# Kernel optimization log

Measured on AMD Instinct MI355X. Metric: run time of the kernel, lower is better.

The kernel has to match this reference:

```python
import jax, jax.numpy as jnp
import numpy as np

N_NODES = 50000
N_EDGES = 800000
DIM = 64
N_HEADS = 4


def setup_inputs() -> dict:
    key = jax.random.key(0)
    ks = jax.random.split(key, 7)
    x = jax.random.normal(ks[0], (N_NODES, DIM), dtype=jnp.float32)
    Wq = jax.random.normal(ks[1], (DIM, DIM), dtype=jnp.float32) / np.sqrt(DIM)
    Wk = jax.random.normal(ks[2], (DIM, DIM), dtype=jnp.float32) / np.sqrt(DIM)
    Wv = jax.random.normal(ks[3], (DIM, DIM), dtype=jnp.float32) / np.sqrt(DIM)
    Wo = jax.random.normal(ks[4], (DIM, DIM), dtype=jnp.float32) / np.sqrt(DIM)
    src = jax.random.randint(ks[5], (N_EDGES,), 0, N_NODES, dtype=jnp.int32)
    dst = jax.random.randint(ks[6], (N_EDGES,), 0, N_NODES, dtype=jnp.int32)
    return {"x": x, "Wq": Wq, "Wk": Wk, "Wv": Wv, "Wo": Wo, "src": src, "dst": dst}


def _scatter_softmax(scores, dst, n_nodes):
    # scores: [E, H]; per-destination-node softmax over incoming edges.
    m = jax.ops.segment_max(scores, dst, num_segments=n_nodes)  # [N, H]
    m = jnp.maximum(m, jnp.float32(-1e9))  # mirror the -1e9 init of the torch code
    ex = jnp.exp(scores - m[dst])  # [E, H]
    denom = jax.ops.segment_sum(ex, dst, num_segments=n_nodes)  # [N, H]
    return ex / (denom[dst] + 1e-9)


def reference(x, Wq, Wk, Wv, Wo, src, dst):
    N, D = x.shape
    H = N_HEADS
    Dh = D // H
    q = (x @ Wq).reshape(N, H, Dh)
    k = (x @ Wk).reshape(N, H, Dh)
    v = (x @ Wv).reshape(N, H, Dh)
    # per-edge attention logits: [E, H]
    scores = jnp.einsum("ehd,ehd->eh", q[dst], k[src]) / jnp.sqrt(jnp.float32(Dh))
    alpha = _scatter_softmax(scores, dst, N)  # [E, H]
    # weighted aggregation of source values onto destination nodes
    agg = jax.ops.segment_sum(alpha[:, :, None] * v[src], dst, num_segments=N)  # [N, H, Dh]
    return agg.reshape(N, D) @ Wo
```

## Files before the change

kernel.cpp:

```cpp
#include <hip/hip_runtime.h>
#include <math.h>

#define HEADS 4
#define DH 16
#define D 64
#define MAXDEG 64

typedef unsigned short ushort_t;
typedef unsigned int uint_t;

__device__ __forceinline__ float bf2f(ushort_t u) {
    return __uint_as_float(((uint_t)u) << 16);
}
__device__ __forceinline__ ushort_t f2bf(float f) {
    uint_t u = __float_as_uint(f);
    u = (u + 0x7FFFu + ((u >> 16) & 1u)) >> 16;
    return (ushort_t)u;
}
__device__ __forceinline__ float bflo(uint_t u) { return __uint_as_float(u << 16); }
__device__ __forceinline__ float bfhi(uint_t u) { return __uint_as_float(u & 0xFFFF0000u); }

__global__ __launch_bounds__(256) void qkv_scatter_kernel(
        const float* __restrict__ x,
        const float* __restrict__ Wq,
        const float* __restrict__ Wk,
        const float* __restrict__ Wv,
        ushort_t* __restrict__ qbf,
        ushort_t* __restrict__ kbf,
        ushort_t* __restrict__ vbf,
        const int* __restrict__ src,
        const int* __restrict__ dst,
        int* __restrict__ cursor,
        ushort_t* __restrict__ csr,
        int N, int E) {
    __shared__ ushort_t wq[D][D];
    __shared__ ushort_t wk[D][D];
    __shared__ ushort_t wv[D][D];
    __shared__ float xs[16][D];

    int tid = threadIdx.x;
    for (int i = tid; i < D * D; i += 256) {
        wq[i >> 6][i & 63] = f2bf(Wq[i]);
        wk[i >> 6][i & 63] = f2bf(Wk[i]);
        wv[i >> 6][i & 63] = f2bf(Wv[i]);
    }

    int c = tid & 63;
    int g = tid >> 6;
    int row = tid >> 4;
    int col4 = tid & 15;

    int ntiles = (N + 15) >> 4;
    for (int tile = blockIdx.x; tile < ntiles; tile += gridDim.x) {
        int n0t = tile * 16;
        __syncthreads();
        float4 xv = make_float4(0.f, 0.f, 0.f, 0.f);
        if (n0t + row < N) xv = *(const float4*)(x + (size_t)(n0t + row) * D + col4 * 4);
        *(float4*)&xs[row][col4 * 4] = xv;
        __syncthreads();

        float aq0=0,aq1=0,aq2=0,aq3=0, ak0=0,ak1=0,ak2=0,ak3=0, av0=0,av1=0,av2=0,av3=0;
#pragma unroll 8
        for (int d = 0; d < D; ++d) {
            float wqv = bf2f(wq[d][c]), wkv = bf2f(wk[d][c]), wvv = bf2f(wv[d][c]);
            float x0 = xs[g*4+0][d], x1 = xs[g*4+1][d], x2 = xs[g*4+2][d], x3 = xs[g*4+3][d];
            aq0 += x0*wqv; ak0 += x0*wkv; av0 += x0*wvv;
            aq1 += x1*wqv; ak1 += x1*wkv; av1 += x1*wvv;
            aq2 += x2*wqv; ak2 += x2*wkv; av2 += x2*wvv;
            aq3 += x3*wqv; ak3 += x3*wkv; av3 += x3*wvv;
        }
        int nb = n0t + g * 4;
        if (nb+0 < N) { qbf[(size_t)(nb+0)*D+c]=f2bf(aq0); kbf[(size_t)(nb+0)*D+c]=f2bf(ak0); vbf[(size_t)(nb+0)*D+c]=f2bf(av0); }
        if (nb+1 < N) { qbf[(size_t)(nb+1)*D+c]=f2bf(aq1); kbf[(size_t)(nb+1)*D+c]=f2bf(ak1); vbf[(size_t)(nb+1)*D+c]=f2bf(av1); }
        if (nb+2 < N) { qbf[(size_t)(nb+2)*D+c]=f2bf(aq2); kbf[(size_t)(nb+2)*D+c]=f2bf(ak2); vbf[(size_t)(nb+2)*D+c]=f2bf(av2); }
        if (nb+3 < N) { qbf[(size_t)(nb+3)*D+c]=f2bf(aq3); kbf[(size_t)(nb+3)*D+c]=f2bf(ak3); vbf[(size_t)(nb+3)*D+c]=f2bf(av3); }
    }

    {
        int e0 = (int)((long long)E * blockIdx.x / gridDim.x);
        int e1 = (int)((long long)E * (blockIdx.x + 1) / gridDim.x);
        for (int e = e0 + tid; e < e1; e += 256) {
            int d = dst[e];
            int s = src[e];
            int pos = atomicAdd(&cursor[d], 1);
            if (pos < MAXDEG) csr[(size_t)d * MAXDEG + pos] = (ushort_t)s;
        }
    }
}

__global__ __launch_bounds__(512) void attn_kernel(const ushort_t* __restrict__ qbf,
                                                   const ushort_t* __restrict__ kbf,
                                                   const ushort_t* __restrict__ vbf,
                                                   const ushort_t* __restrict__ csr,
                                                   const int* __restrict__ cursor,
                                                   const float* __restrict__ Wo,
                                                   float* __restrict__ out,
                                                   int N) {
    __shared__ float wo[D][D];
    __shared__ float aggsh[8][D];

    int tid = threadIdx.x;
    for (int i = tid; i < D * D; i += 512) wo[i >> 6][i & 63] = Wo[i];
    __syncthreads();

    int lane = tid & 63;
    int wave = tid >> 6;
    int node = blockIdx.x * 8 + wave;
    if (node >= N) return;

    int hp  = lane & 3;
    int el  = lane >> 2;
    int hd  = (lane & 31) >> 3;
    int par = lane >> 5;
    int dp2 = 2 * (lane & 31);

    int cnt = cursor[node]; if (cnt > MAXDEG) cnt = MAXDEG;
    const ushort_t* row = csr + (size_t)node * MAXDEG;

    float qr[16];
    {
        const uint4* qp = (const uint4*)(qbf + (size_t)node * D + hp * DH);
        uint4 qa = qp[0], qb = qp[1];
        qr[0]=bflo(qa.x);  qr[1]=bfhi(qa.x);  qr[2]=bflo(qa.y);  qr[3]=bfhi(qa.y);
        qr[4]=bflo(qa.z);  qr[5]=bfhi(qa.z);  qr[6]=bflo(qa.w);  qr[7]=bfhi(qa.w);
        qr[8]=bflo(qb.x);  qr[9]=bfhi(qb.x);  qr[10]=bflo(qb.y); qr[11]=bfhi(qb.y);
        qr[12]=bflo(qb.z); qr[13]=bfhi(qb.z); qr[14]=bflo(qb.w); qr[15]=bfhi(qb.w);
    }

    int s0=0, s1=0, s2=0, s3=0;
    float sc0=-1e30f, sc1=-1e30f, sc2=-1e30f, sc3=-1e30f;

#define PH1SB(sb, sv, scv)                                                      \
    if ((sb) * 16 < cnt) {                                                      \
        int eidx = (sb) * 16 + el;                                              \
        if (eidx < cnt) sv = row[eidx];                                         \
        const uint4* kp = (const uint4*)(kbf + (size_t)sv * D + hp * DH);       \
        uint4 ka = kp[0], kb = kp[1];                                           \
        float dot =                                                             \
          bflo(ka.x)*qr[0]  + bfhi(ka.x)*qr[1]                                  \
        + bflo(ka.y)*qr[2]  + bfhi(ka.y)*qr[3]                                  \
        + bflo(ka.z)*qr[4]  + bfhi(ka.z)*qr[5]                                  \
        + bflo(ka.w)*qr[6]  + bfhi(ka.w)*qr[7]                                  \
        + bflo(kb.x)*qr[8]  + bfhi(kb.x)*qr[9]                                  \
        + bflo(kb.y)*qr[10] + bfhi(kb.y)*qr[11]                                 \
        + bflo(kb.z)*qr[12] + bfhi(kb.z)*qr[13]                                 \
        + bflo(kb.w)*qr[14] + bfhi(kb.w)*qr[15];                                \
        scv = (eidx < cnt) ? dot * 0.25f : -1e30f;                              \
    }
    PH1SB(0, s0, sc0)
    PH1SB(1, s1, sc1)
    PH1SB(2, s2, sc2)
    PH1SB(3, s3, sc3)
#undef PH1SB

    float mloc = fmaxf(fmaxf(sc0, sc1), fmaxf(sc2, sc3));
    mloc = fmaxf(mloc, __shfl_xor(mloc, 4, 64));
    mloc = fmaxf(mloc, __shfl_xor(mloc, 8, 64));
    mloc = fmaxf(mloc, __shfl_xor(mloc, 16, 64));
    mloc = fmaxf(mloc, __shfl_xor(mloc, 32, 64));
    mloc = fmaxf(mloc, -1e9f);

    float pv0 = __expf(sc0 - mloc);
    float pv1 = __expf(sc1 - mloc);
    float pv2 = __expf(sc2 - mloc);
    float pv3 = __expf(sc3 - mloc);
    float ls = (pv0 + pv1) + (pv2 + pv3);
    ls += __shfl_xor(ls, 4, 64);
    ls += __shfl_xor(ls, 8, 64);
    ls += __shfl_xor(ls, 16, 64);
    ls += __shfl_xor(ls, 32, 64);

    float inv = 1.f / (__shfl(ls, hd, 64) + 1e-9f);

    float2 a0 = {0.f, 0.f}, a1 = {0.f, 0.f};
#define PH3SB(sb, sv, pvv)                                                      \
    if ((sb) * 16 < cnt) {                                                      \
        int lim = cnt - (sb) * 16; if (lim > 16) lim = 16;                      \
        for (int e2 = 0; e2 < lim; e2 += 4) {                                   \
            int L0 = 4 * (e2 + par);                                            \
            int ss0 = __shfl(sv, L0, 64);                                       \
            float p0 = __shfl(pvv, L0 + hd, 64);                                \
            uint_t w0 = *(const uint_t*)(vbf + (size_t)ss0 * D + dp2);          \
            a0.x += p0 * bflo(w0);                                              \
            a0.y += p0 * bfhi(w0);                                              \
            int L1 = 4 * (e2 + 2 + par);                                        \
            int ss1 = __shfl(sv, L1, 64);                                       \
            float p1 = __shfl(pvv, L1 + hd, 64);                                \
            uint_t w1 = *(const uint_t*)(vbf + (size_t)ss1 * D + dp2);          \
            a1.x += p1 * bflo(w1);                                              \
            a1.y += p1 * bfhi(w1);                                              \
        }                                                                       \
    }
    PH3SB(0, s0, pv0)
    PH3SB(1, s1, pv1)
    PH3SB(2, s2, pv2)
    PH3SB(3, s3, pv3)
#undef PH3SB

    float ax = a0.x + a1.x, ay = a0.y + a1.y;
    ax += __shfl_xor(ax, 32, 64);
    ay += __shfl_xor(ay, 32, 64);
    if (lane < 32) {
        aggsh[wave][dp2]     = ax * inv;
        aggsh[wave][dp2 + 1] = ay * inv;
    }

    float o = 0.f;
#pragma unroll 8
    for (int d = 0; d < D; ++d) {
        o += aggsh[wave][d] * wo[d][lane];
    }
    out[(size_t)node * D + lane] = o;
}

extern "C" void kernel_launch(void* const* d_in, const int* in_sizes, int n_in,
                              void* d_out, int out_size, void* d_ws, size_t ws_size,
                              hipStream_t stream) {
    const float* x  = (const float*)d_in[0];
    const float* Wq = (const float*)d_in[1];
    const float* Wk = (const float*)d_in[2];
    const float* Wv = (const float*)d_in[3];
    const float* Wo = (const float*)d_in[4];
    const int* src  = (const int*)d_in[5];
    const int* dst  = (const int*)d_in[6];
    float* out = (float*)d_out;

    int N = in_sizes[0] / D;
    int E = in_sizes[5];

    char* ws = (char*)d_ws;
    ushort_t* qbf   = (ushort_t*)ws;  ws += (size_t)N * D * 2;
    ushort_t* kbf   = (ushort_t*)ws;  ws += (size_t)N * D * 2;
    ushort_t* vbf   = (ushort_t*)ws;  ws += (size_t)N * D * 2;
    int* cursor     = (int*)ws;       ws += (size_t)N * 4;
    ushort_t* csr   = (ushort_t*)ws;  ws += (size_t)N * MAXDEG * 2;

    int attnGrid = (N + 7) / 8;

    hipMemsetAsync(cursor, 0, (size_t)N * 4, stream);
    qkv_scatter_kernel<<<2048, 256, 0, stream>>>(x, Wq, Wk, Wv, qbf, kbf, vbf,
                                                 src, dst, cursor, csr, N, E);
    attn_kernel<<<attnGrid, 512, 0, stream>>>(qbf, kbf, vbf, csr, cursor, Wo, out, N);
}
```

Measured before the change: 125.8 us.

## Pre-bucket edges by destination range before CSR scatter for locality

Splits the fused QKV projection plus edge-scatter kernel into three kernels. A new bucketing pass groups edges into 8 destination-range buckets through LDS staging, and a second scatter pass then walks each bucket so that the atomic cursor increments and CSR writes land in a narrower address range, improving L2 locality. This adds an extra read and write of the packed edge list, extra launches, and loses the overlap of the GEMM with the scatter. Packing dst and src into 16 bits each assumes N ≤ 65536, and the fixed per-bucket capacity of E/4 could overflow if dst were skewed.

Result: slower. 145.1 us (+15.3%).

```diff
diff --git a/kernel.cpp b/kernel.cpp
--- a/kernel.cpp
+++ b/kernel.cpp
@@ -5,6 +5,9 @@
 #define DH 16
 #define D 64
 #define MAXDEG 64
+#define NBKT 8
+#define BKT_CAP_LDS 512
+#define SENTINEL 0xFFFFFFFFu
 
 typedef unsigned short ushort_t;
 typedef unsigned int uint_t;
@@ -20,19 +23,61 @@
 __device__ __forceinline__ float bflo(uint_t u) { return __uint_as_float(u << 16); }
 __device__ __forceinline__ float bfhi(uint_t u) { return __uint_as_float(u & 0xFFFF0000u); }
 
-__global__ __launch_bounds__(256) void qkv_scatter_kernel(
-        const float* __restrict__ x,
-        const float* __restrict__ Wq,
-        const float* __restrict__ Wk,
-        const float* __restrict__ Wv,
-        ushort_t* __restrict__ qbf,
-        ushort_t* __restrict__ kbf,
-        ushort_t* __restrict__ vbf,
-        const int* __restrict__ src,
-        const int* __restrict__ dst,
-        int* __restrict__ cursor,
-        ushort_t* __restrict__ csr,
-        int N, int E) {
+__global__ __launch_bounds__(256) void bucket_kernel(const int* __restrict__ src,
+                                                     const int* __restrict__ dst,
+                                                     int* __restrict__ gcur,
+                                                     uint_t* __restrict__ gbkt,
+                                                     int E, int cap, float rb) {
+    __shared__ uint_t bbuf[NBKT][BKT_CAP_LDS];
+    __shared__ int bcnt[NBKT];
+    __shared__ int bbase[NBKT];
+
+    int tid = threadIdx.x;
+    if (tid < NBKT) bcnt[tid] = 0;
+    __syncthreads();
+
+    int e0 = (int)((long long)E * blockIdx.x / gridDim.x);
+    int e1 = (int)((long long)E * (blockIdx.x + 1) / gridDim.x);
+    for (int e = e0 + tid; e < e1; e += 256) {
+        int d = dst[e];
+        int s = src[e];
+        int b = (int)((float)d * rb); if (b > NBKT - 1) b = NBKT - 1;
+        uint_t w = ((uint_t)d << 16) | (uint_t)s;
+        int p = atomicAdd(&bcnt[b], 1);
+        if (p < BKT_CAP_LDS) {
+            bbuf[b][p] = w;
+        } else {
+            int gp = atomicAdd(&gcur[b], 1);
+            gbkt[(size_t)b * cap + gp] = w;
+        }
+    }
+    __syncthreads();
+
+    if (tid < NBKT) {
+        int cnt = bcnt[tid]; if (cnt > BKT_CAP_LDS) cnt = BKT_CAP_LDS;
+        int pad = (cnt + 15) & ~15;
+        for (int i = cnt; i < pad; ++i) bbuf[tid][i] = SENTINEL;
+        bbase[tid] = atomicAdd(&gcur[tid], pad);
+        bcnt[tid] = pad;
+    }
+    __syncthreads();
+
+    for (int b = 0; b < NBKT; ++b) {
+        int cnt = bcnt[b];
+        int base = bbase[b];
+        for (int i = tid; i < cnt; i += 256)
+            gbkt[(size_t)b * cap + base + i] = bbuf[b][i];
+    }
+}
+
+__global__ __launch_bounds__(256) void qkv_kernel(const float* __restrict__ x,
+                                                  const float* __restrict__ Wq,
+                                                  const float* __restrict__ Wk,
+                                                  const float* __restrict__ Wv,
+                                                  ushort_t* __restrict__ qbf,
+                                                  ushort_t* __restrict__ kbf,
+                                                  ushort_t* __restrict__ vbf,
+                                                  int N) {
     __shared__ ushort_t wq[D][D];
     __shared__ ushort_t wk[D][D];
     __shared__ ushort_t wv[D][D];
@@ -75,16 +120,28 @@
         if (nb+2 < N) { qbf[(size_t)(nb+2)*D+c]=f2bf(aq2); kbf[(size_t)(nb+2)*D+c]=f2bf(ak2); vbf[(size_t)(nb+2)*D+c]=f2bf(av2); }
         if (nb+3 < N) { qbf[(size_t)(nb+3)*D+c]=f2bf(aq3); kbf[(size_t)(nb+3)*D+c]=f2bf(ak3); vbf[(size_t)(nb+3)*D+c]=f2bf(av3); }
     }
-
-    {
-        int e0 = (int)((long long)E * blockIdx.x / gridDim.x);
-        int e1 = (int)((long long)E * (blockIdx.x + 1) / gridDim.x);
-        for (int e = e0 + tid; e < e1; e += 256) {
-            int d = dst[e];
-            int s = src[e];
-            int pos = atomicAdd(&cursor[d], 1);
-            if (pos < MAXDEG) csr[(size_t)d * MAXDEG + pos] = (ushort_t)s;
-        }
+}
+
+__global__ __launch_bounds__(256) void scatter2_kernel(const uint_t* __restrict__ gbkt,
+                                                       const int* __restrict__ gcur,
+                                                       int* __restrict__ cursor,
+                                                       ushort_t* __restrict__ csr,
+                                                       int cap) {
+    int g     = blockIdx.x & (NBKT - 1);
+    int chunk = blockIdx.x >> 3;
+    int nch   = gridDim.x >> 3;
+    int cnt = gcur[g];
+    int i0 = (int)((long long)cnt * chunk / nch);
+    int i1 = (int)((long long)cnt * (chunk + 1) / nch);
+    const uint_t* bkt = gbkt + (size_t)g * cap;
+
+    for (int i = i0 + threadIdx.x; i < i1; i += 256) {
+        uint_t w = bkt[i];
+        if (w == SENTINEL) continue;
+        int d = (int)(w >> 16);
+        int s = (int)(w & 0xFFFFu);
+        int pos = atomicAdd(&cursor[d], 1);
+        if (pos < MAXDEG) csr[(size_t)d * MAXDEG + pos] = (ushort_t)s;
     }
 }
 
@@ -227,18 +284,25 @@
 
     int N = in_sizes[0] / D;
     int E = in_sizes[5];
+    int cap = E / 4;
 
     char* ws = (char*)d_ws;
     ushort_t* qbf   = (ushort_t*)ws;  ws += (size_t)N * D * 2;
     ushort_t* kbf   = (ushort_t*)ws;  ws += (size_t)N * D * 2;
     ushort_t* vbf   = (ushort_t*)ws;  ws += (size_t)N * D * 2;
     int* cursor     = (int*)ws;       ws += (size_t)N * 4;
+    int* gcur       = (int*)ws;       ws += 64;
     ushort_t* csr   = (ushort_t*)ws;  ws += (size_t)N * MAXDEG * 2;
-
+    uint_t* gbkt    = (uint_t*)ws;    ws += (size_t)NBKT * cap * 4;
+
+    int nTiles16 = (N + 15) / 16;
+    int gemmGrid = nTiles16 < 2048 ? nTiles16 : 2048;
     int attnGrid = (N + 7) / 8;
-
-    hipMemsetAsync(cursor, 0, (size_t)N * 4, stream);
-    qkv_scatter_kernel<<<2048, 256, 0, stream>>>(x, Wq, Wk, Wv, qbf, kbf, vbf,
-                                                 src, dst, cursor, csr, N, E);
+    float rb = (float)NBKT / (float)N;
+
+    hipMemsetAsync(cursor, 0, (size_t)N * 4 + 64, stream);
+    bucket_kernel<<<1024, 256, 0, stream>>>(src, dst, gcur, gbkt, E, cap, rb);
+    qkv_kernel<<<gemmGrid, 256, 0, stream>>>(x, Wq, Wk, Wv, qbf, kbf, vbf, N);
+    scatter2_kernel<<<2048, 256, 0, stream>>>(gbkt, gcur, cursor, csr, cap);
     attn_kernel<<<attnGrid, 512, 0, stream>>>(qbf, kbf, vbf, csr, cursor, Wo, out, N);
 }
```
